# Kernel tuning notes

Hardware: AMD Instinct MI355X
Metric: run time of the kernel (lower is better)

The kernel has to match this reference:

```python
import jax, jax.numpy as jnp
import numpy as np

B, N, C, F, E, K = 2, 2048, 1024, 4096, 8, 2

def setup_inputs() -> dict:
    key = jax.random.key(0)
    k = jax.random.split(key, 6)
    xavier1 = float(np.sqrt(6.0 / (C + F)))
    xavier2 = float(np.sqrt(6.0 / (F + C)))
    return {
        "x": jax.random.normal(k[0], (B, N, C), dtype=jnp.float32),
        "router_w": jax.random.normal(k[1], (E, C), dtype=jnp.float32) * 0.01,
        "w1": jax.random.uniform(k[2], (E, F, C), dtype=jnp.float32, minval=-xavier1, maxval=xavier1),
        "b1": jnp.zeros((E, F), dtype=jnp.float32),
        "w2": jax.random.uniform(k[3], (E, C, F), dtype=jnp.float32, minval=-xavier2, maxval=xavier2),
        "b2": jnp.zeros((E, C), dtype=jnp.float32),
    }

def reference(x, router_w, w1, b1, w2, b2):
    Bb, Nn, Cc = x.shape
    x_flat = x.reshape(-1, Cc)                                   # [T, C]
    # Router (eval mode: no noise)
    logits = jnp.einsum('tc,ec->te', x_flat, router_w)           # [T, E]
    probs = jax.nn.softmax(logits, axis=-1)
    top_w, top_idx = jax.lax.top_k(probs, K)                     # [T, K]
    top_w = top_w / (jnp.sum(top_w, axis=-1, keepdims=True) + 1e-9)
    # Dense all-expert MLP (same math as the per-expert gather/scatter loop)
    h = jnp.einsum('tc,efc->tef', x_flat, w1) + b1[None]          # [T, E, F]
    h = jax.nn.relu(h)
    y = jnp.einsum('tef,ecf->tec', h, w2) + b2[None]              # [T, E, C]
    # Gather the K selected experts per token and combine
    sel = jnp.take_along_axis(y, top_idx[:, :, None], axis=1)    # [T, K, C]
    out = jnp.einsum('tkc,tk->tc', sel, top_w)                   # [T, C]
    return out.reshape(Bb, Nn, Cc)
```

## Files before the change

### kernel.cpp

```cpp
#include <hip/hip_runtime.h>
#include <hip/hip_fp16.h>


#define T_TOK 4096
#define C_DIM 1024
#define F_DIM 4096
#define E_NUM 8
#define BM 128
#define BN 256
#define BK 64
#define MAXT 72
#define NP   (MAXT * BM)
#define TILE_H 8192

typedef float f32x4 __attribute__((ext_vector_type(4)));
typedef _Float16 half8 __attribute__((ext_vector_type(8)));
typedef _Float16 half4 __attribute__((ext_vector_type(4)));

#define AS1 __attribute__((address_space(1)))
#define AS3 __attribute__((address_space(3)))

__device__ __forceinline__ int swz(int r, int ec) { return ec ^ ((r & 7) << 3); }

__device__ __forceinline__ half8 cvt8(float4 f0, float4 f1) {
  half8 hv;
  hv[0] = (_Float16)f0.x; hv[1] = (_Float16)f0.y; hv[2] = (_Float16)f0.z; hv[3] = (_Float16)f0.w;
  hv[4] = (_Float16)f1.x; hv[5] = (_Float16)f1.y; hv[6] = (_Float16)f1.z; hv[7] = (_Float16)f1.w;
  return hv;
}

__device__ __forceinline__ int xcd_swz(int bid, int nwg) {
  int xcd = bid & 7, rest = bid >> 3;
  int q = nwg >> 3, r = nwg & 7;
  return (xcd < r ? xcd * (q + 1) : r * (q + 1) + (xcd - r) * q) + rest;
}

__global__ __launch_bounds__(256) void router_kernel(
    const float* __restrict__ x, const float* __restrict__ rw,
    int* __restrict__ top_idx, float* __restrict__ top_w)
{
  int t = blockIdx.x * 4 + (threadIdx.x >> 6);
  int lane = threadIdx.x & 63;
  const float* xr = x + (size_t)t * C_DIM;
  float acc[E_NUM];
#pragma unroll
  for (int e = 0; e < E_NUM; ++e) acc[e] = 0.f;
  for (int j = 0; j < C_DIM / 64; ++j) {
    int c = j * 64 + lane;
    float xv = xr[c];
#pragma unroll
    for (int e = 0; e < E_NUM; ++e) acc[e] += xv * rw[e * C_DIM + c];
  }
#pragma unroll
  for (int e = 0; e < E_NUM; ++e) {
    float v = acc[e];
#pragma unroll
    for (int off = 32; off > 0; off >>= 1) v += __shfl_xor(v, off);
    acc[e] = v;
  }
  if (lane == 0) {
    float mx = acc[0];
    for (int e = 1; e < E_NUM; ++e) mx = fmaxf(mx, acc[e]);
    float p[E_NUM]; float Z = 0.f;
    for (int e = 0; e < E_NUM; ++e) { p[e] = expf(acc[e] - mx); Z += p[e]; }
    int b0 = 0;
    for (int e = 1; e < E_NUM; ++e) if (p[e] > p[b0]) b0 = e;
    int b1i = -1; float pb = -1.f;
    for (int e = 0; e < E_NUM; ++e) if (e != b0 && p[e] > pb) { pb = p[e]; b1i = e; }
    float p0 = p[b0] / Z, p1 = pb / Z;
    float s = p0 + p1 + 1e-9f;
    top_idx[t * 2 + 0] = b0;
    top_idx[t * 2 + 1] = b1i;
    top_w[t * 2 + 0] = p0 / s;
    top_w[t * 2 + 1] = p1 / s;
  }
}

__global__ void build_lists(const int* __restrict__ top_idx,
                            int* __restrict__ rows_g, int* __restrict__ counts,
                            int* __restrict__ tile_off, int* __restrict__ inv)
{
  int e = threadIdx.x >> 6;
  int lane = threadIdx.x & 63;
  int cnt = 0;
  for (int t0 = 0; t0 < T_TOK; t0 += 64) {
    int t = t0 + lane;
    bool sel = (top_idx[t * 2] == e) || (top_idx[t * 2 + 1] == e);
    cnt += __popcll(__ballot(sel));
  }
  if (lane == 0) counts[e] = cnt;
  __syncthreads();
  if (threadIdx.x == 0) {
    int o = 0;
    for (int i = 0; i < E_NUM; ++i) { tile_off[i] = o; o += (counts[i] + BM - 1) / BM; }
    tile_off[E_NUM] = o;
  }
  __syncthreads();
  int base = tile_off[e] * BM;
  int pos = 0;
  for (int t0 = 0; t0 < T_TOK; t0 += 64) {
    int t = t0 + lane;
    int i0 = top_idx[t * 2], i1 = top_idx[t * 2 + 1];
    bool sel = (i0 == e) || (i1 == e);
    unsigned long long mask = __ballot(sel);
    if (sel) {
      int p = pos + __popcll(mask & ((1ull << lane) - 1ull));
      int slot = t * 2 + ((i0 == e) ? 0 : 1);
      rows_g[base + p] = slot;
      inv[slot] = (e << 16) | (base + p);
    }
    pos += __popcll(mask);
  }
}

__global__ __launch_bounds__(256) void gather_x(
    const float* __restrict__ x, const int* __restrict__ rows_g,
    const int* __restrict__ counts, const int* __restrict__ tile_off,
    _Float16* __restrict__ xg)
{
  unsigned g = blockIdx.x * 256 + threadIdx.x;
  unsigned p = g >> 7, ccr = g & 127;
  int gt = p >> 7, r = p & 127;
  int kc = ccr >> 3, c8 = ccr & 7;
  int e = -1;
#pragma unroll
  for (int i = 0; i < E_NUM; ++i)
    if (gt >= tile_off[i] && gt < tile_off[i + 1]) e = i;
  half8 hv = {};
  if (e >= 0) {
    int nrem = counts[e] - (gt - tile_off[e]) * BM;
    if (r < nrem) {
      int t = rows_g[p] >> 1;
      const float4* s = reinterpret_cast<const float4*>(x + (size_t)t * C_DIM + kc * 64 + c8 * 8);
      hv = cvt8(s[0], s[1]);
    }
  }
  *reinterpret_cast<half8*>(xg + ((size_t)gt * 16 + kc) * TILE_H + r * 64 + ((c8 ^ (r & 7)) << 3)) = hv;
}

__global__ __launch_bounds__(256) void cvt_w(
    const float* __restrict__ w1, const float* __restrict__ w2,
    _Float16* __restrict__ w1t, _Float16* __restrict__ w2t,
    int ch, int Fc, int lgnftl, int lgnkc, unsigned halfChunks)
{
  unsigned g = blockIdx.x * 256 + threadIdx.x;
  if (g < halfChunks) {
    unsigned tile = g >> 10;
    unsigned kc = tile & 15;
    unsigned et = tile >> 4;
    unsigned ftl = et & ((1u << lgnftl) - 1);
    unsigned e = et >> lgnftl;
    unsigned r = (g >> 3) & 127;
    unsigned sc = g & 7;
    unsigned c8 = sc ^ (r & 7);
    unsigned frow = ftl * 128 + r;
    const float4* s = reinterpret_cast<const float4*>(
        w1 + ((size_t)e * F_DIM + ch * Fc + frow) * C_DIM + kc * 64 + c8 * 8);
    *reinterpret_cast<half8*>(w1t + (size_t)g * 8) = cvt8(s[0], s[1]);
  } else {
    unsigned g2 = g - halfChunks;
    unsigned tile = g2 >> 10;
    unsigned kc = tile & ((1u << lgnkc) - 1);
    unsigned et = tile >> lgnkc;
    unsigned ct = et & 7;
    unsigned e = et >> 3;
    unsigned r = (g2 >> 3) & 127;
    unsigned sc = g2 & 7;
    unsigned c8 = sc ^ (r & 7);
    unsigned c = ct * 128 + r;
    const float4* s = reinterpret_cast<const float4*>(
        w2 + ((size_t)e * C_DIM + c) * F_DIM + ch * Fc + kc * 64 + c8 * 8);
    *reinterpret_cast<half8*>(w2t + (size_t)g2 * 8) = cvt8(s[0], s[1]);
  }
}

#define STAGE_TILE(aSrc_, b0Src_, b1Src_)                                         \
  {                                                                               \
    _Pragma("unroll")                                                             \
    for (int i_ = 0; i_ < 2; ++i_) {                                              \
      int o_ = tid * 8 + i_ * 4096;                                               \
      __builtin_amdgcn_global_load_lds((const AS1 void*)((aSrc_) + o_),           \
          (AS3 void*)(&As[o_]), 16, 0, 0);                                        \
      __builtin_amdgcn_global_load_lds((const AS1 void*)((b0Src_) + o_),          \
          (AS3 void*)(&Bs[o_]), 16, 0, 0);                                        \
      __builtin_amdgcn_global_load_lds((const AS1 void*)((b1Src_) + o_),          \
          (AS3 void*)(&Bs[8192 + o_]), 16, 0, 0);                                 \
    }                                                                             \
  }

#define COMPUTE_TILE()                                                            \
  _Pragma("unroll")                                                               \
  for (int kk = 0; kk < BK; kk += 32) {                                           \
    const int klo = kk + (lane >> 4) * 8;                                         \
    half8 aF[4], bF[4];                                                           \
    _Pragma("unroll")                                                             \
    for (int m = 0; m < 4; ++m) {                                                 \
      int r = wr * 64 + m * 16 + (lane & 15);                                     \
      aF[m] = *reinterpret_cast<const half8*>(&As[r * BK + swz(r, klo)]);         \
    }                                                                             \
    _Pragma("unroll")                                                             \
    for (int n = 0; n < 4; ++n) {                                                 \
      int br = wc * 64 + n * 16 + (lane & 15);                                    \
      bF[n] = *reinterpret_cast<const half8*>(                                    \
          &Bs[(br >> 7) * 8192 + (br & 127) * 64 + swz(br, klo)]);                \
    }                                                                             \
    _Pragma("unroll")                                                             \
    for (int m = 0; m < 4; ++m)                                                   \
      _Pragma("unroll")                                                           \
      for (int n = 0; n < 4; ++n)                                                 \
        acc[m][n] = __builtin_amdgcn_mfma_f32_16x16x32_f16(bF[n], aF[m], acc[m][n], 0, 0, 0); \
  }

#define STAGE2(aSrc_, bSrc_)                                                      \
  {                                                                               \
    _Pragma("unroll")                                                             \
    for (int i_ = 0; i_ < 4; ++i_) {                                              \
      int o_ = tid * 8 + i_ * 2048;                                               \
      __builtin_amdgcn_global_load_lds((const AS1 void*)((aSrc_) + o_),           \
          (AS3 void*)(&As[o_]), 16, 0, 0);                                        \
      __builtin_amdgcn_global_load_lds((const AS1 void*)((bSrc_) + o_),           \
          (AS3 void*)(&Bs[o_]), 16, 0, 0);                                        \
    }                                                                             \
  }

#define COMPUTE2()                                                                \
  _Pragma("unroll")                                                               \
  for (int kk = 0; kk < BK; kk += 32) {                                           \
    const int klo = kk + (lane >> 4) * 8;                                         \
    half8 aF[4], bF[4];                                                           \
    _Pragma("unroll")                                                             \
    for (int m = 0; m < 4; ++m) {                                                 \
      int r = wr * 64 + m * 16 + (lane & 15);                                     \
      aF[m] = *reinterpret_cast<const half8*>(&As[r * BK + swz(r, klo)]);         \
    }                                                                             \
    _Pragma("unroll")                                                             \
    for (int n = 0; n < 4; ++n) {                                                 \
      int r = wc * 64 + n * 16 + (lane & 15);                                     \
      bF[n] = *reinterpret_cast<const half8*>(&Bs[r * BK + swz(r, klo)]);         \
    }                                                                             \
    _Pragma("unroll")                                                             \
    for (int m = 0; m < 4; ++m)                                                   \
      _Pragma("unroll")                                                           \
      for (int n = 0; n < 4; ++n)                                                 \
        acc[m][n] = __builtin_amdgcn_mfma_f32_16x16x32_f16(bF[n], aF[m], acc[m][n], 0, 0, 0); \
  }

__global__ __launch_bounds__(512) void gemm1_kernel(
    const _Float16* __restrict__ xg, const _Float16* __restrict__ w1t,
    const float* __restrict__ b1, const int* __restrict__ counts,
    const int* __restrict__ tile_off, _Float16* __restrict__ ht,
    int ch, int Fc)
{
  const int NFT = Fc / BN;
  const int wgid = xcd_swz(blockIdx.x, gridDim.x);
  const int grp = wgid / (8 * NFT);
  const int rem = wgid - grp * 8 * NFT;
  const int ft = rem >> 3;
  const int gt = grp * 8 + (rem & 7);
  if (gt >= tile_off[E_NUM]) return;
  int e = 0;
  while (gt >= tile_off[e + 1]) ++e;
  const int nftl = Fc >> 7;
  const _Float16* At  = xg + (size_t)gt * 16 * TILE_H;
  const _Float16* Bt0 = w1t + (size_t)(e * nftl + 2 * ft) * 16 * TILE_H;
  const _Float16* Bt1 = w1t + (size_t)(e * nftl + 2 * ft + 1) * 16 * TILE_H;

  __shared__ __align__(16) _Float16 As[TILE_H];
  __shared__ __align__(16) _Float16 Bs[2 * TILE_H];

  const int tid = threadIdx.x;
  const int lane = tid & 63;
  const int wave = tid >> 6;
  const int wr = wave >> 2, wc = wave & 3;

  f32x4 acc[4][4];
#pragma unroll
  for (int m = 0; m < 4; ++m)
#pragma unroll
    for (int n = 0; n < 4; ++n) acc[m][n] = (f32x4){0.f, 0.f, 0.f, 0.f};

  for (int kc = 0; kc < 16; ++kc) {
    STAGE_TILE(At + (size_t)kc * TILE_H, Bt0 + (size_t)kc * TILE_H, Bt1 + (size_t)kc * TILE_H);
    __syncthreads();
    COMPUTE_TILE();
    __syncthreads();
  }

  const int nkcF = Fc >> 6;
  const float* b1e = b1 + e * F_DIM + ch * Fc;
#pragma unroll
  for (int m = 0; m < 4; ++m) {
    int tok = wr * 64 + m * 16 + (lane & 15);
#pragma unroll
    for (int n = 0; n < 4; ++n) {
      int flb = ft * BN + wc * 64 + n * 16 + ((lane >> 4) << 2);
      float4 bv = *reinterpret_cast<const float4*>(b1e + flb);
      half4 hv;
      hv[0] = (_Float16)fmaxf(acc[m][n][0] + bv.x, 0.f);
      hv[1] = (_Float16)fmaxf(acc[m][n][1] + bv.y, 0.f);
      hv[2] = (_Float16)fmaxf(acc[m][n][2] + bv.z, 0.f);
      hv[3] = (_Float16)fmaxf(acc[m][n][3] + bv.w, 0.f);
      *reinterpret_cast<half4*>(
          ht + ((size_t)gt * nkcF + (flb >> 6)) * TILE_H + tok * 64 +
          ((((flb >> 3) & 7) ^ (tok & 7)) << 3) + (flb & 7)) = hv;
    }
  }
}

__global__ __launch_bounds__(256) void gemm2_kernel(
    const _Float16* __restrict__ ht, const _Float16* __restrict__ w2t,
    const int* __restrict__ tile_off, _Float16* __restrict__ y,
    int Fc, int kspl, int accum)
{
  const int NCMB = 8 * kspl;
  const int wgid = xcd_swz(blockIdx.x, gridDim.x);
  const int grp = wgid / (8 * NCMB);
  const int rem = wgid - grp * 8 * NCMB;
  const int cmb = rem >> 3;
  const int gt = grp * 8 + (rem & 7);
  if (gt >= tile_off[E_NUM]) return;
  const int ct = cmb & 7;
  const int ks = cmb >> 3;
  int e = 0;
  while (gt >= tile_off[e + 1]) ++e;
  const int nkc = Fc >> 6;
  const int klen = nkc / kspl;
  const _Float16* At = ht + ((size_t)gt * nkc + ks * klen) * TILE_H;
  const _Float16* Bt = w2t + ((size_t)(e * 8 + ct) * nkc + ks * klen) * TILE_H;

  __shared__ __align__(16) _Float16 As[TILE_H];
  __shared__ __align__(16) _Float16 Bs[TILE_H];

  const int tid = threadIdx.x;
  const int lane = tid & 63;
  const int wave = tid >> 6;
  const int wr = wave >> 1, wc = wave & 1;

  f32x4 acc[4][4];
#pragma unroll
  for (int m = 0; m < 4; ++m)
#pragma unroll
    for (int n = 0; n < 4; ++n) acc[m][n] = (f32x4){0.f, 0.f, 0.f, 0.f};

  for (int kc = 0; kc < klen; ++kc) {
    STAGE2(At + (size_t)kc * TILE_H, Bt + (size_t)kc * TILE_H);
    __syncthreads();
    COMPUTE2();
    __syncthreads();
  }

  _Float16* yk = y + ((size_t)(ks * MAXT + gt) * BM) * C_DIM;
#pragma unroll
  for (int m = 0; m < 4; ++m) {
    int pos = wr * 64 + m * 16 + (lane & 15);
#pragma unroll
    for (int n = 0; n < 4; ++n) {
      int cb = ct * 128 + wc * 64 + n * 16 + ((lane >> 4) << 2);
      half4* p = reinterpret_cast<half4*>(yk + (size_t)pos * C_DIM + cb);
      half4 hv;
      if (accum) {
        half4 old = *p;
        hv[0] = (_Float16)(acc[m][n][0] + (float)old[0]);
        hv[1] = (_Float16)(acc[m][n][1] + (float)old[1]);
        hv[2] = (_Float16)(acc[m][n][2] + (float)old[2]);
        hv[3] = (_Float16)(acc[m][n][3] + (float)old[3]);
      } else {
        hv[0] = (_Float16)acc[m][n][0];
        hv[1] = (_Float16)acc[m][n][1];
        hv[2] = (_Float16)acc[m][n][2];
        hv[3] = (_Float16)acc[m][n][3];
      }
      *p = hv;
    }
  }
}

__global__ __launch_bounds__(256) void combine_kernel(
    const _Float16* __restrict__ y, const int* __restrict__ inv,
    const float* __restrict__ top_w, const float* __restrict__ b2,
    float* __restrict__ out, int kspl)
{
  int g = blockIdx.x * 256 + threadIdx.x;
  int t = g >> 7, c8 = (g & 127) << 3;
  float o[8];
#pragma unroll
  for (int i = 0; i < 8; ++i) o[i] = 0.f;
#pragma unroll
  for (int k = 0; k < 2; ++k) {
    int iv = inv[t * 2 + k];
    int e = iv >> 16, pos = iv & 0xffff;
    float w = top_w[t * 2 + k];
    const float4* bb = reinterpret_cast<const float4*>(b2 + e * C_DIM + c8);
    float4 bv0 = bb[0], bv1 = bb[1];
    float s[8] = {bv0.x, bv0.y, bv0.z, bv0.w, bv1.x, bv1.y, bv1.z, bv1.w};
    for (int ks = 0; ks < kspl; ++ks) {
      half8 hv = *reinterpret_cast<const half8*>(
          y + ((size_t)(ks * MAXT * BM + pos)) * C_DIM + c8);
#pragma unroll
      for (int i = 0; i < 8; ++i) s[i] += (float)hv[i];
    }
#pragma unroll
    for (int i = 0; i < 8; ++i) o[i] += w * s[i];
  }
  float4* op = reinterpret_cast<float4*>(out + (size_t)t * C_DIM + c8);
  op[0] = (float4){o[0], o[1], o[2], o[3]};
  op[1] = (float4){o[4], o[5], o[6], o[7]};
}

extern "C" void kernel_launch(void* const* d_in, const int* in_sizes, int n_in,
                              void* d_out, int out_size, void* d_ws, size_t ws_size,
                              hipStream_t stream)
{
  const float* x  = (const float*)d_in[0];
  const float* rw = (const float*)d_in[1];
  const float* w1 = (const float*)d_in[2];
  const float* b1 = (const float*)d_in[3];
  const float* w2 = (const float*)d_in[4];
  const float* b2 = (const float*)d_in[5];
  float* out = (float*)d_out;

  char* ws = (char*)d_ws;
  size_t off = 0;
  auto carve = [&](size_t bytes) -> void* {
    void* p = ws + off;
    off += (bytes + 255) & ~(size_t)255;
    return p;
  };
  int*   top_idx  = (int*)carve((size_t)T_TOK * 2 * sizeof(int));
  float* top_w    = (float*)carve((size_t)T_TOK * 2 * sizeof(float));
  int*   counts   = (int*)carve(E_NUM * sizeof(int));
  int*   tile_off = (int*)carve((E_NUM + 1) * sizeof(int));
  int*   rows_g   = (int*)carve((size_t)NP * sizeof(int));
  int*   inv      = (int*)carve((size_t)T_TOK * 2 * sizeof(int));
  _Float16* xg    = (_Float16*)carve((size_t)MAXT * 16 * TILE_H * sizeof(_Float16));
  _Float16* y     = (_Float16*)carve((size_t)2 * NP * C_DIM * sizeof(_Float16));
  size_t fixed = off;

  int nchunk = 8;
  const int cands[4] = {1, 2, 4, 8};
  for (int ci = 0; ci < 4; ++ci) {
    int n = cands[ci];
    size_t fc = (size_t)(F_DIM / n);
    size_t w1b = ((size_t)E_NUM * fc * C_DIM * 2 + 255) & ~(size_t)255;
    size_t w2b = ((size_t)E_NUM * C_DIM * fc * 2 + 255) & ~(size_t)255;
    size_t htb = ((size_t)MAXT * (fc >> 6) * TILE_H * 2 + 255) & ~(size_t)255;
    if (fixed + w1b + w2b + htb <= ws_size) { nchunk = n; break; }
  }
  const int Fc = F_DIM / nchunk;
  int lgFc = 0; while ((1 << lgFc) < Fc) ++lgFc;
  _Float16* w1t = (_Float16*)carve((size_t)E_NUM * Fc * C_DIM * sizeof(_Float16));
  _Float16* w2t = (_Float16*)carve((size_t)E_NUM * C_DIM * Fc * sizeof(_Float16));
  _Float16* ht  = (_Float16*)carve((size_t)MAXT * (Fc >> 6) * TILE_H * sizeof(_Float16));

  const int kspl = (Fc >= 2048) ? 2 : 1;

  router_kernel<<<T_TOK / 4, 256, 0, stream>>>(x, rw, top_idx, top_w);
  build_lists<<<1, 512, 0, stream>>>(top_idx, rows_g, counts, tile_off, inv);
  gather_x<<<(MAXT * BM * 128) / 256, 256, 0, stream>>>(x, rows_g, counts, tile_off, xg);

  const unsigned halfChunks = (unsigned)Fc << 10;
  for (int ch = 0; ch < nchunk; ++ch) {
    cvt_w<<<8 * Fc, 256, 0, stream>>>(w1, w2, w1t, w2t, ch, Fc, lgFc - 7, lgFc - 6, halfChunks);
    gemm1_kernel<<<MAXT * (Fc / BN), 512, 0, stream>>>(
        xg, w1t, b1, counts, tile_off, ht, ch, Fc);
    gemm2_kernel<<<MAXT * 8 * kspl, 256, 0, stream>>>(
        ht, w2t, tile_off, y, Fc, kspl, ch != 0);
  }
  combine_kernel<<<(T_TOK * 128) / 256, 256, 0, stream>>>(y, inv, top_w, b2, out, kspl);
}
```

Baseline: 352.7 us.

## Enlarge both expert GEMMs to 256x256 tiles with paired token tiles

Both grouped GEMMs now use 256x256 block tiles. Each block stages two 128-row token tiles and two 128-row weight tiles per K step, and eight waves each compute a 128x64 sub-tile. Expert token counts are rounded up to multiples of 256, so MAXT grows to 80. The intent is to halve weight and activation reloads per output and raise MFMA work per LDS stage. The cost is more padding waste, 64 KB of LDS, larger accumulator register pressure (launch_bounds 512,2), and fewer blocks to fill the GPU.

```diff
diff --git a/kernel.cpp b/kernel.cpp
--- a/kernel.cpp
+++ b/kernel.cpp
@@ -6,11 +6,8 @@
 #define C_DIM 1024
 #define F_DIM 4096
 #define E_NUM 8
-#define BM 128
-#define BN 256
-#define BK 64
-#define MAXT 72
-#define NP   (MAXT * BM)
+#define MAXT 80
+#define NP   (MAXT * 128)
 #define TILE_H 8192
 
 typedef float f32x4 __attribute__((ext_vector_type(4)));
@@ -92,11 +89,11 @@
   __syncthreads();
   if (threadIdx.x == 0) {
     int o = 0;
-    for (int i = 0; i < E_NUM; ++i) { tile_off[i] = o; o += (counts[i] + BM - 1) / BM; }
+    for (int i = 0; i < E_NUM; ++i) { tile_off[i] = o; o += 2 * ((counts[i] + 255) >> 8); }
     tile_off[E_NUM] = o;
   }
   __syncthreads();
-  int base = tile_off[e] * BM;
+  int base = tile_off[e] * 128;
   int pos = 0;
   for (int t0 = 0; t0 < T_TOK; t0 += 64) {
     int t = t0 + lane;
@@ -128,7 +125,7 @@
     if (gt >= tile_off[i] && gt < tile_off[i + 1]) e = i;
   half8 hv = {};
   if (e >= 0) {
-    int nrem = counts[e] - (gt - tile_off[e]) * BM;
+    int nrem = counts[e] - (gt - tile_off[e]) * 128;
     if (r < nrem) {
       int t = rows_g[p] >> 1;
       const float4* s = reinterpret_cast<const float4*>(x + (size_t)t * C_DIM + kc * 64 + c8 * 8);
@@ -174,98 +171,65 @@
   }
 }
 
-#define STAGE_TILE(aSrc_, b0Src_, b1Src_)                                         \
+#define STAGE4(a0_, a1_, b0_, b1_)                                                \
   {                                                                               \
     _Pragma("unroll")                                                             \
     for (int i_ = 0; i_ < 2; ++i_) {                                              \
       int o_ = tid * 8 + i_ * 4096;                                               \
-      __builtin_amdgcn_global_load_lds((const AS1 void*)((aSrc_) + o_),           \
+      __builtin_amdgcn_global_load_lds((const AS1 void*)((a0_) + o_),             \
           (AS3 void*)(&As[o_]), 16, 0, 0);                                        \
-      __builtin_amdgcn_global_load_lds((const AS1 void*)((b0Src_) + o_),          \
+      __builtin_amdgcn_global_load_lds((const AS1 void*)((a1_) + o_),             \
+          (AS3 void*)(&As[8192 + o_]), 16, 0, 0);                                 \
+      __builtin_amdgcn_global_load_lds((const AS1 void*)((b0_) + o_),             \
           (AS3 void*)(&Bs[o_]), 16, 0, 0);                                        \
-      __builtin_amdgcn_global_load_lds((const AS1 void*)((b1Src_) + o_),          \
+      __builtin_amdgcn_global_load_lds((const AS1 void*)((b1_) + o_),             \
           (AS3 void*)(&Bs[8192 + o_]), 16, 0, 0);                                 \
     }                                                                             \
   }
 
-#define COMPUTE_TILE()                                                            \
+#define COMPUTE256()                                                              \
   _Pragma("unroll")                                                               \
-  for (int kk = 0; kk < BK; kk += 32) {                                           \
+  for (int kk = 0; kk < 64; kk += 32) {                                           \
     const int klo = kk + (lane >> 4) * 8;                                         \
-    half8 aF[4], bF[4];                                                           \
+    half8 aF[8], bF[4];                                                           \
     _Pragma("unroll")                                                             \
-    for (int m = 0; m < 4; ++m) {                                                 \
-      int r = wr * 64 + m * 16 + (lane & 15);                                     \
-      aF[m] = *reinterpret_cast<const half8*>(&As[r * BK + swz(r, klo)]);         \
+    for (int m = 0; m < 8; ++m) {                                                 \
+      int r = m * 16 + (lane & 15);                                               \
+      aF[m] = *reinterpret_cast<const half8*>(&As[wr * 8192 + r * 64 + swz(r, klo)]); \
     }                                                                             \
     _Pragma("unroll")                                                             \
     for (int n = 0; n < 4; ++n) {                                                 \
-      int br = wc * 64 + n * 16 + (lane & 15);                                    \
-      bF[n] = *reinterpret_cast<const half8*>(                                    \
-          &Bs[(br >> 7) * 8192 + (br & 127) * 64 + swz(br, klo)]);                \
+      int rb = (wc & 1) * 64 + n * 16 + (lane & 15);                              \
+      bF[n] = *reinterpret_cast<const half8*>(&Bs[(wc >> 1) * 8192 + rb * 64 + swz(rb, klo)]); \
     }                                                                             \
     _Pragma("unroll")                                                             \
-    for (int m = 0; m < 4; ++m)                                                   \
+    for (int m = 0; m < 8; ++m)                                                   \
       _Pragma("unroll")                                                           \
       for (int n = 0; n < 4; ++n)                                                 \
         acc[m][n] = __builtin_amdgcn_mfma_f32_16x16x32_f16(bF[n], aF[m], acc[m][n], 0, 0, 0); \
   }
 
-#define STAGE2(aSrc_, bSrc_)                                                      \
-  {                                                                               \
-    _Pragma("unroll")                                                             \
-    for (int i_ = 0; i_ < 4; ++i_) {                                              \
-      int o_ = tid * 8 + i_ * 2048;                                               \
-      __builtin_amdgcn_global_load_lds((const AS1 void*)((aSrc_) + o_),           \
-          (AS3 void*)(&As[o_]), 16, 0, 0);                                        \
-      __builtin_amdgcn_global_load_lds((const AS1 void*)((bSrc_) + o_),           \
-          (AS3 void*)(&Bs[o_]), 16, 0, 0);                                        \
-    }                                                                             \
-  }
-
-#define COMPUTE2()                                                                \
-  _Pragma("unroll")                                                               \
-  for (int kk = 0; kk < BK; kk += 32) {                                           \
-    const int klo = kk + (lane >> 4) * 8;                                         \
-    half8 aF[4], bF[4];                                                           \
-    _Pragma("unroll")                                                             \
-    for (int m = 0; m < 4; ++m) {                                                 \
-      int r = wr * 64 + m * 16 + (lane & 15);                                     \
-      aF[m] = *reinterpret_cast<const half8*>(&As[r * BK + swz(r, klo)]);         \
-    }                                                                             \
-    _Pragma("unroll")                                                             \
-    for (int n = 0; n < 4; ++n) {                                                 \
-      int r = wc * 64 + n * 16 + (lane & 15);                                     \
-      bF[n] = *reinterpret_cast<const half8*>(&Bs[r * BK + swz(r, klo)]);         \
-    }                                                                             \
-    _Pragma("unroll")                                                             \
-    for (int m = 0; m < 4; ++m)                                                   \
-      _Pragma("unroll")                                                           \
-      for (int n = 0; n < 4; ++n)                                                 \
-        acc[m][n] = __builtin_amdgcn_mfma_f32_16x16x32_f16(bF[n], aF[m], acc[m][n], 0, 0, 0); \
-  }
-
-__global__ __launch_bounds__(512) void gemm1_kernel(
+__global__ __launch_bounds__(512, 2) void gemm1_kernel(
     const _Float16* __restrict__ xg, const _Float16* __restrict__ w1t,
-    const float* __restrict__ b1, const int* __restrict__ counts,
-    const int* __restrict__ tile_off, _Float16* __restrict__ ht,
-    int ch, int Fc)
-{
-  const int NFT = Fc / BN;
+    const float* __restrict__ b1, const int* __restrict__ tile_off,
+    _Float16* __restrict__ ht, int ch, int Fc)
+{
+  const int NFT = Fc >> 8;
   const int wgid = xcd_swz(blockIdx.x, gridDim.x);
-  const int grp = wgid / (8 * NFT);
-  const int rem = wgid - grp * 8 * NFT;
-  const int ft = rem >> 3;
-  const int gt = grp * 8 + (rem & 7);
+  const int grp = wgid / (4 * NFT);
+  const int rem = wgid - grp * 4 * NFT;
+  const int ft = rem >> 2;
+  const int gt = (grp * 4 + (rem & 3)) * 2;
   if (gt >= tile_off[E_NUM]) return;
   int e = 0;
   while (gt >= tile_off[e + 1]) ++e;
   const int nftl = Fc >> 7;
-  const _Float16* At  = xg + (size_t)gt * 16 * TILE_H;
+  const _Float16* At0 = xg + (size_t)gt * 16 * TILE_H;
+  const _Float16* At1 = xg + (size_t)(gt + 1) * 16 * TILE_H;
   const _Float16* Bt0 = w1t + (size_t)(e * nftl + 2 * ft) * 16 * TILE_H;
   const _Float16* Bt1 = w1t + (size_t)(e * nftl + 2 * ft + 1) * 16 * TILE_H;
 
-  __shared__ __align__(16) _Float16 As[TILE_H];
+  __shared__ __align__(16) _Float16 As[2 * TILE_H];
   __shared__ __align__(16) _Float16 Bs[2 * TILE_H];
 
   const int tid = threadIdx.x;
@@ -273,27 +237,29 @@
   const int wave = tid >> 6;
   const int wr = wave >> 2, wc = wave & 3;
 
-  f32x4 acc[4][4];
-#pragma unroll
-  for (int m = 0; m < 4; ++m)
+  f32x4 acc[8][4];
+#pragma unroll
+  for (int m = 0; m < 8; ++m)
 #pragma unroll
     for (int n = 0; n < 4; ++n) acc[m][n] = (f32x4){0.f, 0.f, 0.f, 0.f};
 
   for (int kc = 0; kc < 16; ++kc) {
-    STAGE_TILE(At + (size_t)kc * TILE_H, Bt0 + (size_t)kc * TILE_H, Bt1 + (size_t)kc * TILE_H);
+    size_t ko = (size_t)kc * TILE_H;
+    STAGE4(At0 + ko, At1 + ko, Bt0 + ko, Bt1 + ko);
     __syncthreads();
-    COMPUTE_TILE();
+    COMPUTE256();
     __syncthreads();
   }
 
   const int nkcF = Fc >> 6;
+  const int gtw = gt + wr;
   const float* b1e = b1 + e * F_DIM + ch * Fc;
 #pragma unroll
-  for (int m = 0; m < 4; ++m) {
-    int tok = wr * 64 + m * 16 + (lane & 15);
+  for (int m = 0; m < 8; ++m) {
+    int tok = m * 16 + (lane & 15);
 #pragma unroll
     for (int n = 0; n < 4; ++n) {
-      int flb = ft * BN + wc * 64 + n * 16 + ((lane >> 4) << 2);
+      int flb = ft * 256 + wc * 64 + n * 16 + ((lane >> 4) << 2);
       float4 bv = *reinterpret_cast<const float4*>(b1e + flb);
       half4 hv;
       hv[0] = (_Float16)fmaxf(acc[m][n][0] + bv.x, 0.f);
@@ -301,62 +267,65 @@
       hv[2] = (_Float16)fmaxf(acc[m][n][2] + bv.z, 0.f);
       hv[3] = (_Float16)fmaxf(acc[m][n][3] + bv.w, 0.f);
       *reinterpret_cast<half4*>(
-          ht + ((size_t)gt * nkcF + (flb >> 6)) * TILE_H + tok * 64 +
+          ht + ((size_t)gtw * nkcF + (flb >> 6)) * TILE_H + tok * 64 +
           ((((flb >> 3) & 7) ^ (tok & 7)) << 3) + (flb & 7)) = hv;
     }
   }
 }
 
-__global__ __launch_bounds__(256) void gemm2_kernel(
+__global__ __launch_bounds__(512, 2) void gemm2_kernel(
     const _Float16* __restrict__ ht, const _Float16* __restrict__ w2t,
     const int* __restrict__ tile_off, _Float16* __restrict__ y,
     int Fc, int kspl, int accum)
 {
-  const int NCMB = 8 * kspl;
   const int wgid = xcd_swz(blockIdx.x, gridDim.x);
-  const int grp = wgid / (8 * NCMB);
-  const int rem = wgid - grp * 8 * NCMB;
-  const int cmb = rem >> 3;
-  const int gt = grp * 8 + (rem & 7);
+  const int NCMB = 4 * kspl;
+  const int grp = wgid / (4 * NCMB);
+  const int rem = wgid - grp * 4 * NCMB;
+  const int cmb = rem >> 2;
+  const int gt = (grp * 4 + (rem & 3)) * 2;
   if (gt >= tile_off[E_NUM]) return;
-  const int ct = cmb & 7;
-  const int ks = cmb >> 3;
+  const int ct2 = cmb & 3;
+  const int ks = cmb >> 2;
   int e = 0;
   while (gt >= tile_off[e + 1]) ++e;
   const int nkc = Fc >> 6;
   const int klen = nkc / kspl;
-  const _Float16* At = ht + ((size_t)gt * nkc + ks * klen) * TILE_H;
-  const _Float16* Bt = w2t + ((size_t)(e * 8 + ct) * nkc + ks * klen) * TILE_H;
-
-  __shared__ __align__(16) _Float16 As[TILE_H];
-  __shared__ __align__(16) _Float16 Bs[TILE_H];
+  const _Float16* At0 = ht + ((size_t)gt * nkc + ks * klen) * TILE_H;
+  const _Float16* At1 = ht + ((size_t)(gt + 1) * nkc + ks * klen) * TILE_H;
+  const _Float16* Bt0 = w2t + ((size_t)(e * 8 + 2 * ct2) * nkc + ks * klen) * TILE_H;
+  const _Float16* Bt1 = w2t + ((size_t)(e * 8 + 2 * ct2 + 1) * nkc + ks * klen) * TILE_H;
+
+  __shared__ __align__(16) _Float16 As[2 * TILE_H];
+  __shared__ __align__(16) _Float16 Bs[2 * TILE_H];
 
   const int tid = threadIdx.x;
   const int lane = tid & 63;
   const int wave = tid >> 6;
-  const int wr = wave >> 1, wc = wave & 1;
-
-  f32x4 acc[4][4];
-#pragma unroll
-  for (int m = 0; m < 4; ++m)
+  const int wr = wave >> 2, wc = wave & 3;
+
+  f32x4 acc[8][4];
+#pragma unroll
+  for (int m = 0; m < 8; ++m)
 #pragma unroll
     for (int n = 0; n < 4; ++n) acc[m][n] = (f32x4){0.f, 0.f, 0.f, 0.f};
 
   for (int kc = 0; kc < klen; ++kc) {
-    STAGE2(At + (size_t)kc * TILE_H, Bt + (size_t)kc * TILE_H);
+    size_t ko = (size_t)kc * TILE_H;
+    STAGE4(At0 + ko, At1 + ko, Bt0 + ko, Bt1 + ko);
     __syncthreads();
-    COMPUTE2();
+    COMPUTE256();
     __syncthreads();
   }
 
-  _Float16* yk = y + ((size_t)(ks * MAXT + gt) * BM) * C_DIM;
-#pragma unroll
-  for (int m = 0; m < 4; ++m) {
-    int pos = wr * 64 + m * 16 + (lane & 15);
+  _Float16* yk = y + ((size_t)(ks * MAXT + gt + wr) * 128) * C_DIM;
+#pragma unroll
+  for (int m = 0; m < 8; ++m) {
+    int tok = m * 16 + (lane & 15);
 #pragma unroll
     for (int n = 0; n < 4; ++n) {
-      int cb = ct * 128 + wc * 64 + n * 16 + ((lane >> 4) << 2);
-      half4* p = reinterpret_cast<half4*>(yk + (size_t)pos * C_DIM + cb);
+      int cb = ct2 * 256 + wc * 64 + n * 16 + ((lane >> 4) << 2);
+      half4* p = reinterpret_cast<half4*>(yk + (size_t)tok * C_DIM + cb);
       half4 hv;
       if (accum) {
         half4 old = *p;
@@ -395,7 +364,7 @@
     float s[8] = {bv0.x, bv0.y, bv0.z, bv0.w, bv1.x, bv1.y, bv1.z, bv1.w};
     for (int ks = 0; ks < kspl; ++ks) {
       half8 hv = *reinterpret_cast<const half8*>(
-          y + ((size_t)(ks * MAXT * BM + pos)) * C_DIM + c8);
+          y + ((size_t)(ks * MAXT * 128 + pos)) * C_DIM + c8);
 #pragma unroll
       for (int i = 0; i < 8; ++i) s[i] += (float)hv[i];
     }
@@ -456,14 +425,14 @@
 
   router_kernel<<<T_TOK / 4, 256, 0, stream>>>(x, rw, top_idx, top_w);
   build_lists<<<1, 512, 0, stream>>>(top_idx, rows_g, counts, tile_off, inv);
-  gather_x<<<(MAXT * BM * 128) / 256, 256, 0, stream>>>(x, rows_g, counts, tile_off, xg);
+  gather_x<<<(MAXT * 128 * 128) / 256, 256, 0, stream>>>(x, rows_g, counts, tile_off, xg);
 
   const unsigned halfChunks = (unsigned)Fc << 10;
   for (int ch = 0; ch < nchunk; ++ch) {
     cvt_w<<<8 * Fc, 256, 0, stream>>>(w1, w2, w1t, w2t, ch, Fc, lgFc - 7, lgFc - 6, halfChunks);
-    gemm1_kernel<<<MAXT * (Fc / BN), 512, 0, stream>>>(
-        xg, w1t, b1, counts, tile_off, ht, ch, Fc);
-    gemm2_kernel<<<MAXT * 8 * kspl, 256, 0, stream>>>(
+    gemm1_kernel<<<(MAXT / 2) * (Fc / 256), 512, 0, stream>>>(
+        xg, w1t, b1, tile_off, ht, ch, Fc);
+    gemm2_kernel<<<(MAXT / 2) * 4 * kspl, 512, 0, stream>>>(
         ht, w2t, tile_off, y, Fc, kspl, ch != 0);
   }
   combine_kernel<<<(T_TOK * 128) / 256, 256, 0, stream>>>(y, inv, top_w, b2, out, kspl);
```

After: 431.6 us. 1.22x slower.
